# Kernel tuning notes

Hardware: AMD Instinct MI355X
Metric: run time of the kernel (lower is better)

Reference implementation:

```python
import jax, jax.numpy as jnp
import numpy as np

B, C, W, H = 4, 256, 64, 64

def setup_inputs() -> dict:
    key = jax.random.key(0)
    ks = jax.random.split(key, 6)
    return {
        "fm_source": jax.random.normal(ks[0], (B, C, W, H), dtype=jnp.float32),
        "fm_reference": jax.random.normal(ks[1], (B, C, W, H), dtype=jnp.float32),
        "w_lambda": jax.random.normal(ks[2], (1, C, 1, 1), dtype=jnp.float32) * 0.05,
        "b_lambda": jax.random.normal(ks[3], (1,), dtype=jnp.float32) * 0.05,
        "w_beta": jax.random.normal(ks[4], (1, C, 1, 1), dtype=jnp.float32) * 0.05,
        "b_beta": jax.random.normal(ks[5], (1,), dtype=jnp.float32) * 0.05,
    }

def reference(fm_source, fm_reference, w_lambda, b_lambda, w_beta, b_beta):
    b, c, w, h = fm_reference.shape
    n = w * h
    # 1x1 convs on the reference feature map -> per-pixel scalars, flattened to [B, N]
    wl = w_lambda.reshape(c)
    wb = w_beta.reshape(c)
    ref_flat = fm_reference.reshape(b, c, n)   # [B, C, N]
    src_flat = fm_source.reshape(b, c, n)      # [B, C, N]
    old_lambda = jnp.einsum("bcn,c->bn", ref_flat, wl) + b_lambda[0]  # [B, N]
    old_beta = jnp.einsum("bcn,c->bn", ref_flat, wb) + b_beta[0]      # [B, N]
    # energy[b, i, j] = <src pixel i, ref pixel j> over channels
    energy = jnp.einsum("bci,bcj->bij", src_flat, ref_flat)  # [B, N, N]
    attention = jax.nn.softmax(energy, axis=-1)              # softmax over ref pixels j
    # new_lambda[b, i] = sum_j old_lambda[b, j] * attention[b, i, j]
    new_lambda = jnp.einsum("bj,bij->bi", old_lambda, attention).reshape(b, 1, w, h)
    new_beta = jnp.einsum("bj,bij->bi", old_beta, attention).reshape(b, 1, w, h)
    # broadcast modulation over the 256 channels
    return new_lambda * fm_source + new_beta
```

## Files before the change

kernel.cpp:

```cpp
#include <hip/hip_runtime.h>


#define B_ 4
#define C_ 256
#define N_ 4096
#define LOG2E 1.44269504f
#define SHIFT2 86.5617f
#define JSLICE 8
#define BN_ (B_ * N_)
#define NT_ 16
#define NBUF 3

typedef _Float16 half_t;
typedef _Float16 v8h  __attribute__((ext_vector_type(8)));
typedef float    v16f __attribute__((ext_vector_type(16)));

#define GLDS16(g, l) __builtin_amdgcn_global_load_lds(                         \
    (const __attribute__((address_space(1))) void*)(g),                        \
    (__attribute__((address_space(3))) void*)(l), 16, 0, 0)

__global__ void k_prep(const float* __restrict__ src,
                       const float* __restrict__ ref,
                       const float* __restrict__ wl, const float* __restrict__ bl,
                       const float* __restrict__ wb, const float* __restrict__ bb,
                       half_t* __restrict__ s16, half_t* __restrict__ r16,
                       float* __restrict__ oldL, float* __restrict__ oldB) {
    if (blockIdx.z == 8) {
        int b  = blockIdx.y;
        int n0 = blockIdx.x * 64;
        int nl = threadIdx.x & 63;
        int cq = threadIdx.x >> 6;
        const float* p = ref + ((size_t)b * C_ + cq * 64) * N_ + n0 + nl;
        float aL = 0.f, aB = 0.f;
#pragma unroll 8
        for (int c = 0; c < 64; c++) {
            float v = p[(size_t)c * N_];
            aL += v * wl[cq * 64 + c];
            aB += v * wb[cq * 64 + c];
        }
        __shared__ float red[8][64];
        red[cq][nl]     = aL;
        red[4 + cq][nl] = aB;
        __syncthreads();
        if (threadIdx.x < 64) {
            int t = threadIdx.x;
            oldL[(size_t)b * N_ + n0 + t] =
                red[0][t] + red[1][t] + red[2][t] + red[3][t] + bl[0];
        } else if (threadIdx.x < 128) {
            int t = threadIdx.x - 64;
            oldB[(size_t)b * N_ + n0 + t] =
                red[4][t] + red[5][t] + red[6][t] + red[7][t] + bb[0];
        }
        return;
    }
    __shared__ float tile[64][65];
    int z  = blockIdx.z;
    int b  = z & 3;
    const float* in  = (z < B_) ? src : ref;
    half_t*      out = (z < B_) ? s16 : r16;
    float scale      = (z < B_) ? LOG2E : 1.0f;
    int c0 = blockIdx.y * 64;
    int n0 = blockIdx.x * 64;
    int tx = threadIdx.x & 15, ty = threadIdx.x >> 4;
#pragma unroll
    for (int q = 0; q < 4; q++) {
        int c = ty + q * 16;
        float4 v = *(const float4*)(in + ((size_t)b * C_ + c0 + c) * N_ + n0 + tx * 4);
        tile[c][tx * 4 + 0] = v.x;
        tile[c][tx * 4 + 1] = v.y;
        tile[c][tx * 4 + 2] = v.z;
        tile[c][tx * 4 + 3] = v.w;
    }
    __syncthreads();
    int r   = threadIdx.x & 31;
    int lhi = (threadIdx.x >> 5) & 1;
    int wv  = threadIdx.x >> 6;
#pragma unroll
    for (int nt = 0; nt < 2; nt++) {
        int nl = nt * 32 + r;
        v8h o;
#pragma unroll
        for (int e = 0; e < 8; e++)
            o[e] = (half_t)(tile[wv * 16 + lhi * 8 + e][nl] * scale);
        size_t tj = (size_t)(n0 >> 5) + nt;
        size_t kb = (size_t)(c0 >> 4) + wv;
        *(v8h*)(out + ((((size_t)b * 128 + tj) * 16 + kb) * 64 + (threadIdx.x & 63)) * 8) = o;
    }
}

__global__ __launch_bounds__(512, 2) void k_flash(
        const half_t* __restrict__ sT, const half_t* __restrict__ rT,
        const float* __restrict__ oldL, const float* __restrict__ oldB,
        float* __restrict__ part ) {
    __shared__ half_t lds[NBUF][8192];
    __shared__ float oL[512], oB[512];
    int bid    = blockIdx.x;
    int b      = bid & 3;
    int jslice = (bid >> 2) & (JSLICE - 1);
    int iblock = bid >> 5;
    int tid    = threadIdx.x;
    int wv     = tid >> 6;
    int lane   = tid & 63;
    int l31    = lane & 31, lhi = lane >> 5;
    int ti     = iblock * 8 + wv;
    int i0     = ti * 32;
    int j0     = jslice * (N_ / JSLICE);
    int tj0    = j0 >> 5;

    const half_t* aP = sT + (((size_t)b * 128 + ti) * 16) * 512 + (size_t)lane * 8;
    v8h a[16];
#pragma unroll
    for (int kb = 0; kb < 16; kb++) a[kb] = *(const v8h*)(aP + (size_t)kb * 512);

    oL[tid] = oldL[(size_t)b * N_ + j0 + tid];
    oB[tid] = oldB[(size_t)b * N_ + j0 + tid];

    const half_t* bBase = rT + (((size_t)b * 128 + tj0) * 16) * 512;

    float sp[16], sl[16], sb[16];
#pragma unroll
    for (int r = 0; r < 16; r++) { sp[r] = 0.f; sl[r] = 0.f; sb[r] = 0.f; }

#pragma unroll
    for (int t = 0; t < 2; t++)
#pragma unroll
        for (int q = 0; q < 2; q++) {
            int chunk = q * 8 + wv;
            GLDS16(bBase + (size_t)t * 8192 + (size_t)chunk * 512 + (size_t)lane * 8,
                   &lds[t][(size_t)chunk * 512]);
        }
    __syncthreads();

    for (int jt = 0; jt < NT_; jt++) {
        if (jt < NT_ - 1) asm volatile("s_waitcnt vmcnt(2)" ::: "memory");
        else              asm volatile("s_waitcnt vmcnt(0)" ::: "memory");
        __builtin_amdgcn_s_barrier();
        __builtin_amdgcn_sched_barrier(0);
        if (jt + 2 < NT_) {
            const half_t* g = bBase + (size_t)(jt + 2) * 8192;
            half_t* dst = &lds[(jt + 2) % NBUF][0];
#pragma unroll
            for (int q = 0; q < 2; q++) {
                int chunk = q * 8 + wv;
                GLDS16(g + (size_t)chunk * 512 + (size_t)lane * 8,
                       dst + (size_t)chunk * 512);
            }
        }
        const half_t* bt = &lds[jt % NBUF][0] + (size_t)lane * 8;
        float lam = oL[jt * 32 + l31];
        float bet = oB[jt * 32 + l31];
        v16f acc0, acc1;
#pragma unroll
        for (int r = 0; r < 16; r++) { acc0[r] = -SHIFT2; acc1[r] = 0.f; }
#pragma unroll
        for (int kb = 0; kb < 8; kb++) {
            acc0 = __builtin_amdgcn_mfma_f32_32x32x16_f16(
                a[kb],     *(const v8h*)(bt + (size_t)kb * 512),       acc0, 0, 0, 0);
            acc1 = __builtin_amdgcn_mfma_f32_32x32x16_f16(
                a[kb + 8], *(const v8h*)(bt + (size_t)(kb + 8) * 512), acc1, 0, 0, 0);
        }
#pragma unroll
        for (int r = 0; r < 16; r++) {
            float p = __builtin_amdgcn_exp2f(acc0[r] + acc1[r]);
            sp[r] += p;
            sl[r] += p * lam;
            sb[r] += p * bet;
        }
    }

    float* pSP = part + ((size_t)jslice * 3 + 0) * BN_;
    float* pSL = part + ((size_t)jslice * 3 + 1) * BN_;
    float* pSB = part + ((size_t)jslice * 3 + 2) * BN_;
#pragma unroll
    for (int r = 0; r < 16; r++) {
        float tp = sp[r], tl = sl[r], tb = sb[r];
#pragma unroll
        for (int m = 1; m <= 16; m <<= 1) {
            tp += __shfl_xor(tp, m, 64);
            tl += __shfl_xor(tl, m, 64);
            tb += __shfl_xor(tb, m, 64);
        }
        if (l31 == 0) {
            int row = (r & 3) + 8 * (r >> 2) + 4 * lhi;
            size_t ig = (size_t)b * N_ + i0 + row;
            pSP[ig] = tp; pSL[ig] = tl; pSB[ig] = tb;
        }
    }
}

__global__ void k_comb(const float* __restrict__ part,
                       float* __restrict__ newLT ) {
    int g = blockIdx.x * 256 + threadIdx.x;
    float sp = 0.f, sl = 0.f, sb = 0.f;
#pragma unroll
    for (int s = 0; s < JSLICE; s++) {
        sp += part[((size_t)s * 3 + 0) * BN_ + g];
        sl += part[((size_t)s * 3 + 1) * BN_ + g];
        sb += part[((size_t)s * 3 + 2) * BN_ + g];
    }
    newLT[g]       = sl / sp;
    newLT[BN_ + g] = sb / sp;
}

__global__ void k_post(const float* __restrict__ src,
                       const float* __restrict__ newLT,
                       float* __restrict__ out) {
    int b  = blockIdx.x;
    int n0 = blockIdx.y * 1024;
    int c0 = blockIdx.z * 4;
    int t  = threadIdx.x;
    size_t bn = (size_t)b * N_ + n0 + t * 4;
    float4 L = *(const float4*)(newLT + bn);
    float4 T = *(const float4*)(newLT + BN_ + bn);
    const float* sp0 = src + ((size_t)b * C_ + c0) * N_ + n0 + t * 4;
    float*       op0 = out + ((size_t)b * C_ + c0) * N_ + n0 + t * 4;
#pragma unroll
    for (int c = 0; c < 4; c++) {
        float4 v = *(const float4*)(sp0 + (size_t)c * N_);
        float4 o;
        o.x = L.x * v.x + T.x;
        o.y = L.y * v.y + T.y;
        o.z = L.z * v.z + T.z;
        o.w = L.w * v.w + T.w;
        *(float4*)(op0 + (size_t)c * N_) = o;
    }
}

extern "C" void kernel_launch(void* const* d_in, const int* in_sizes, int n_in,
                              void* d_out, int out_size, void* d_ws, size_t ws_size,
                              hipStream_t stream) {
    const float* src = (const float*)d_in[0];
    const float* ref = (const float*)d_in[1];
    const float* wl  = (const float*)d_in[2];
    const float* bl  = (const float*)d_in[3];
    const float* wb  = (const float*)d_in[4];
    const float* bb  = (const float*)d_in[5];
    float* out = (float*)d_out;

    float* oldL  = (float*)d_ws;
    float* oldB  = oldL + BN_;
    float* part  = oldB + BN_;
    float* newLT = part + (size_t)3 * JSLICE * BN_;
    size_t needF  = ((size_t)2 + 3 * JSLICE + 2) * BN_ * sizeof(float);
    size_t need16 = (size_t)2 * B_ * N_ * C_ * sizeof(half_t);
    half_t* s16;
    if (ws_size >= needF + need16) s16 = (half_t*)((char*)d_ws + needF);
    else                           s16 = (half_t*)d_out;
    half_t* r16 = s16 + (size_t)B_ * N_ * C_;

    k_prep<<<dim3(N_ / 64, C_ / 64, 9), 256, 0, stream>>>(
        src, ref, wl, bl, wb, bb, s16, r16, oldL, oldB);
    k_flash<<<512, 512, 0, stream>>>(s16, r16, oldL, oldB, part);
    k_comb<<<BN_ / 256, 256, 0, stream>>>(part, newLT);
    k_post<<<dim3(B_, N_ / 1024, C_ / 4), 256, 0, stream>>>(src, newLT, out);
}
```

Baseline: 146.7 us.

## Software-pipeline exp/accumulate of previous tile with MFMAs of current tile

Restructures the flash loop so the exp2 and softmax-sum accumulation for the previous tile are interleaved with the MFMA issue of the current tile, using ping-pong accumulator sets. The LDS ring shrinks from three buffers to two with a plain __syncthreads per tile, and the lambda/beta values are read straight from global memory instead of being staged in LDS. The aim is to hide transcendental and VALU work behind matrix-core latency, at the cost of more live registers (two accumulator pairs) and a shorter prefetch distance.

```diff
diff --git a/kernel.cpp b/kernel.cpp
--- a/kernel.cpp
+++ b/kernel.cpp
@@ -9,7 +9,6 @@
 #define JSLICE 8
 #define BN_ (B_ * N_)
 #define NT_ 16
-#define NBUF 3
 
 typedef _Float16 half_t;
 typedef _Float16 v8h  __attribute__((ext_vector_type(8)));
@@ -18,6 +17,39 @@
 #define GLDS16(g, l) __builtin_amdgcn_global_load_lds(                         \
     (const __attribute__((address_space(1))) void*)(g),                        \
     (__attribute__((address_space(3))) void*)(l), 16, 0, 0)
+
+#define TILE_SEC(T, ACC0, ACC1, LAM, BET, DO_FIN, FACC0, FACC1, FLAM, FBET)    \
+  {                                                                            \
+    __syncthreads();                                                           \
+    if ((T) + 1 < NT_) {                                                       \
+      const half_t* g = bBase + (size_t)((T) + 1) * 8192;                      \
+      _Pragma("unroll")                                                        \
+      for (int q = 0; q < 2; q++) {                                            \
+        int chunk = q * 8 + wv;                                                \
+        GLDS16(g + (size_t)chunk * 512 + (size_t)lane * 8,                     \
+               &lds[((T) + 1) & 1][(size_t)chunk * 512]);                      \
+      }                                                                        \
+    }                                                                          \
+    LAM = oLp[(T) * 32];                                                       \
+    BET = oBp[(T) * 32];                                                       \
+    const half_t* bt = lds[(T) & 1] + (size_t)lane * 8;                        \
+    _Pragma("unroll")                                                          \
+    for (int r = 0; r < 16; r++) { ACC0[r] = -SHIFT2; ACC1[r] = 0.f; }         \
+    _Pragma("unroll")                                                          \
+    for (int kb = 0; kb < 8; kb++) {                                           \
+      ACC0 = __builtin_amdgcn_mfma_f32_32x32x16_f16(                           \
+          a[kb], *(const v8h*)(bt + (size_t)kb * 512), ACC0, 0, 0, 0);         \
+      ACC1 = __builtin_amdgcn_mfma_f32_32x32x16_f16(                           \
+          a[kb + 8], *(const v8h*)(bt + (size_t)(kb + 8) * 512), ACC1, 0,0,0); \
+      if (DO_FIN) {                                                            \
+        _Pragma("unroll")                                                      \
+        for (int rr = 2 * kb; rr < 2 * kb + 2; rr++) {                         \
+          float p = __builtin_amdgcn_exp2f(FACC0[rr] + FACC1[rr]);             \
+          sp[rr] += p; sl[rr] += p * FLAM; sb[rr] += p * FBET;                 \
+        }                                                                      \
+      }                                                                        \
+    }                                                                          \
+  }
 
 __global__ void k_prep(const float* __restrict__ src,
                        const float* __restrict__ ref,
@@ -92,8 +124,7 @@
         const half_t* __restrict__ sT, const half_t* __restrict__ rT,
         const float* __restrict__ oldL, const float* __restrict__ oldB,
         float* __restrict__ part ) {
-    __shared__ half_t lds[NBUF][8192];
-    __shared__ float oL[512], oB[512];
+    __shared__ half_t lds[2][8192];
     int bid    = blockIdx.x;
     int b      = bid & 3;
     int jslice = (bid >> 2) & (JSLICE - 1);
@@ -112,60 +143,35 @@
 #pragma unroll
     for (int kb = 0; kb < 16; kb++) a[kb] = *(const v8h*)(aP + (size_t)kb * 512);
 
-    oL[tid] = oldL[(size_t)b * N_ + j0 + tid];
-    oB[tid] = oldB[(size_t)b * N_ + j0 + tid];
-
     const half_t* bBase = rT + (((size_t)b * 128 + tj0) * 16) * 512;
+    const float*  oLp = oldL + (size_t)b * N_ + j0 + l31;
+    const float*  oBp = oldB + (size_t)b * N_ + j0 + l31;
 
     float sp[16], sl[16], sb[16];
 #pragma unroll
     for (int r = 0; r < 16; r++) { sp[r] = 0.f; sl[r] = 0.f; sb[r] = 0.f; }
 
 #pragma unroll
-    for (int t = 0; t < 2; t++)
-#pragma unroll
-        for (int q = 0; q < 2; q++) {
-            int chunk = q * 8 + wv;
-            GLDS16(bBase + (size_t)t * 8192 + (size_t)chunk * 512 + (size_t)lane * 8,
-                   &lds[t][(size_t)chunk * 512]);
-        }
-    __syncthreads();
-
-    for (int jt = 0; jt < NT_; jt++) {
-        if (jt < NT_ - 1) asm volatile("s_waitcnt vmcnt(2)" ::: "memory");
-        else              asm volatile("s_waitcnt vmcnt(0)" ::: "memory");
-        __builtin_amdgcn_s_barrier();
-        __builtin_amdgcn_sched_barrier(0);
-        if (jt + 2 < NT_) {
-            const half_t* g = bBase + (size_t)(jt + 2) * 8192;
-            half_t* dst = &lds[(jt + 2) % NBUF][0];
-#pragma unroll
-            for (int q = 0; q < 2; q++) {
-                int chunk = q * 8 + wv;
-                GLDS16(g + (size_t)chunk * 512 + (size_t)lane * 8,
-                       dst + (size_t)chunk * 512);
-            }
-        }
-        const half_t* bt = &lds[jt % NBUF][0] + (size_t)lane * 8;
-        float lam = oL[jt * 32 + l31];
-        float bet = oB[jt * 32 + l31];
-        v16f acc0, acc1;
-#pragma unroll
-        for (int r = 0; r < 16; r++) { acc0[r] = -SHIFT2; acc1[r] = 0.f; }
-#pragma unroll
-        for (int kb = 0; kb < 8; kb++) {
-            acc0 = __builtin_amdgcn_mfma_f32_32x32x16_f16(
-                a[kb],     *(const v8h*)(bt + (size_t)kb * 512),       acc0, 0, 0, 0);
-            acc1 = __builtin_amdgcn_mfma_f32_32x32x16_f16(
-                a[kb + 8], *(const v8h*)(bt + (size_t)(kb + 8) * 512), acc1, 0, 0, 0);
-        }
-#pragma unroll
-        for (int r = 0; r < 16; r++) {
-            float p = __builtin_amdgcn_exp2f(acc0[r] + acc1[r]);
-            sp[r] += p;
-            sl[r] += p * lam;
-            sb[r] += p * bet;
-        }
+    for (int q = 0; q < 2; q++) {
+        int chunk = q * 8 + wv;
+        GLDS16(bBase + (size_t)chunk * 512 + (size_t)lane * 8,
+               &lds[0][(size_t)chunk * 512]);
+    }
+
+    v16f accA0, accA1, accB0, accB1;
+    float lamA = 0.f, betA = 0.f, lamB = 0.f, betB = 0.f;
+
+    TILE_SEC(0, accA0, accA1, lamA, betA, false, accB0, accB1, lamB, betB)
+    for (int pt = 0; pt < 7; pt++) {
+        int t1 = 2 * pt + 1, t2 = 2 * pt + 2;
+        TILE_SEC(t1, accB0, accB1, lamB, betB, true, accA0, accA1, lamA, betA)
+        TILE_SEC(t2, accA0, accA1, lamA, betA, true, accB0, accB1, lamB, betB)
+    }
+    TILE_SEC(15, accB0, accB1, lamB, betB, true, accA0, accA1, lamA, betA)
+#pragma unroll
+    for (int r = 0; r < 16; r++) {
+        float p = __builtin_amdgcn_exp2f(accB0[r] + accB1[r]);
+        sp[r] += p; sl[r] += p * lamB; sb[r] += p * betB;
     }
 
     float* pSP = part + ((size_t)jslice * 3 + 0) * BN_;
```

New measurement: 145.4 us. About the same (-0.9%).
